# Performance work log

Measured on AMD Instinct MI355X. Metric: run time of the kernel, lower is better.

## Reference

```python
import jax, jax.numpy as jnp
import numpy as np

B, TC, TP = 2, 1024, 512
NVC, NVP = 8, 4
D, K, H, DFF, L, HOR, NQ = 128, 3, 8, 512, 2, 96, 3
DK = D // H
MASK_VAL = -1e4  # finite stand-in for -inf; entmax15 support never reaches entries this far below the row max


def entmax15(z):
    # Exact 1.5-entmax over the last axis (Peters & Martins sort-based algorithm).
    z = z / 2.0
    z = z - jnp.max(z, axis=-1, keepdims=True)
    zs = jnp.flip(jnp.sort(z, axis=-1), axis=-1)  # descending
    kk = jnp.arange(1, z.shape[-1] + 1, dtype=z.dtype)
    mean = jnp.cumsum(zs, axis=-1) / kk
    meansq = jnp.cumsum(zs * zs, axis=-1) / kk
    ss = kk * (meansq - mean * mean)
    delta = (1.0 - ss) / kk
    pos = delta > 0
    sqrt_d = jnp.where(pos, jnp.sqrt(jnp.where(pos, delta, 1.0)), 0.0)  # grad-safe sqrt
    tau = mean - sqrt_d
    support = jnp.sum((tau <= zs).astype(jnp.int32), axis=-1, keepdims=True)
    tau_star = jnp.take_along_axis(tau, support - 1, axis=-1)
    return jnp.square(jnp.clip(z - tau_star, 0.0, None))


def layer_norm(x, g, b, eps=1e-5):
    m = jnp.mean(x, axis=-1, keepdims=True)
    v = jnp.mean(jnp.square(x - m), axis=-1, keepdims=True)
    return (x - m) * jax.lax.rsqrt(v + eps) * g + b


def selector(x, conv_w, conv_b, sel_w, sel_b, key):
    # x: [B, T, nv]; causal depthwise-grouped conv -> per-var local states [B, T, nv, D]
    Bs, T, nv = x.shape
    xc = jnp.transpose(x, (0, 2, 1))  # [B, nv, T]
    out = jax.lax.conv_general_dilated(
        xc, conv_w, window_strides=(1,), padding=[(K - 1, 0)],
        dimension_numbers=('NCH', 'OIH', 'NCH'), feature_group_count=nv)
    ls = out.reshape(Bs, nv, D, T) + conv_b[None, :, :, None]
    ls = jnp.transpose(ls, (0, 3, 1, 2))  # [B, T, nv, D]
    scores = ls @ sel_w + sel_b  # [B, T, nv]
    scores = jnp.clip(scores, -10.0, 10.0)
    scores = scores + 1e-4 * jax.random.normal(key, scores.shape, scores.dtype)
    w = entmax15(scores)  # [B, T, nv]
    weighted = jnp.sum(ls * w[..., None], axis=2)  # [B, T, D]
    return weighted, w


def attn_block(x, Wq, bq, Wk, bk, Wv, bv, Wo, bo):
    Bs, T, _ = x.shape
    q = (x @ Wq + bq).reshape(Bs, T, H, DK)
    k = (x @ Wk + bk).reshape(Bs, T, H, DK)
    v = (x @ Wv + bv).reshape(Bs, T, H, DK)
    scores = jnp.einsum('bthd,bshd->bhts', q, k) / jnp.sqrt(jnp.float32(DK))
    mask = jnp.triu(jnp.ones((T, T), bool), 1)
    scores = jnp.where(mask[None, None], MASK_VAL, scores)
    w = entmax15(scores)            # [B, H, T, T]
    w_avg = jnp.mean(w, axis=1)     # [B, T, T]
    v_comb = jnp.mean(v, axis=2)    # [B, T, DK]
    out = jnp.einsum('bts,bsd->btd', w_avg, v_comb)
    return out @ Wo + bo, w_avg


def forward(x_cond, x_pred, cw_c, cb_c, sw_c, sb_c, cw_p, cb_p, sw_p, sb_p,
            Wq, bq, Wk, bk, Wv, bv, Wo, bo, ln1_g, ln1_b,
            fw1, fb1, fw2, fb2, ln2_g, ln2_b, proj_w, proj_b):
    nk = jax.random.key(42)
    xc, v_cond = selector(x_cond, cw_c, cb_c, sw_c, sb_c, jax.random.fold_in(nk, 0))
    xp, v_pred = selector(x_pred, cw_p, cb_p, sw_p, sb_p, jax.random.fold_in(nk, 1))
    x = jnp.concatenate([xc, xp], axis=1)  # [B, TC+TP, D]
    logs = []
    for l in range(L):
        a, w = attn_block(x, Wq[l], bq[l], Wk[l], bk[l], Wv[l], bv[l], Wo[l], bo[l])
        x = layer_norm(x + a, ln1_g[l], ln1_b[l])
        h = jax.nn.relu(x @ fw1[l] + fb1[l])
        x = layer_norm(h @ fw2[l] + fb2[l] + x, ln2_g[l], ln2_b[l])
        logs.append(w)
    seq_last = x[:, -1, :]
    out = jnp.einsum('bd,qdh->bqh', seq_last, proj_w) + proj_b  # [B, NQ, HOR]
    return out, v_cond, v_pred, jnp.stack(logs)


def setup_inputs():
    key = jax.random.key(0)
    ks = jax.random.split(key, 16)
    def w(i, shp):
        return (0.02 * jax.random.normal(ks[i], shp)).astype(jnp.float32)
    z = lambda shp: jnp.zeros(shp, jnp.float32)
    o = lambda shp: jnp.ones(shp, jnp.float32)
    return {
        'x_cond': jax.random.normal(ks[0], (B, TC, NVC), jnp.float32),
        'x_pred': jax.random.normal(ks[1], (B, TP, NVP), jnp.float32),
        'cw_c': w(2, (NVC * D, 1, K)), 'cb_c': z((NVC, D)),
        'sw_c': w(3, (D,)), 'sb_c': z((1,)),
        'cw_p': w(4, (NVP * D, 1, K)), 'cb_p': z((NVP, D)),
        'sw_p': w(5, (D,)), 'sb_p': z((1,)),
        'Wq': w(6, (L, D, D)), 'bq': z((L, D)),
        'Wk': w(7, (L, D, D)), 'bk': z((L, D)),
        'Wv': w(8, (L, D, D)), 'bv': z((L, D)),
        'Wo': w(9, (L, DK, D)), 'bo': z((L, D)),
        'ln1_g': o((L, D)), 'ln1_b': z((L, D)),
        'fw1': w(10, (L, D, DFF)), 'fb1': z((L, DFF)),
        'fw2': w(11, (L, DFF, D)), 'fb2': z((L, D)),
        'ln2_g': o((L, D)), 'ln2_b': z((L, D)),
        'proj_w': w(12, (NQ, D, HOR)), 'proj_b': z((NQ, HOR)),
    }


def reference(x_cond, x_pred, cw_c, cb_c, sw_c, sb_c, cw_p, cb_p, sw_p, sb_p,
              Wq, bq, Wk, bk, Wv, bv, Wo, bo, ln1_g, ln1_b,
              fw1, fb1, fw2, fb2, ln2_g, ln2_b, proj_w, proj_b):
    return forward(x_cond, x_pred, cw_c, cb_c, sw_c, sb_c, cw_p, cb_p, sw_p, sb_p,
                   Wq, bq, Wk, bk, Wv, bv, Wo, bo, ln1_g, ln1_b,
                   fw1, fb1, fw2, fb2, ln2_g, ln2_b, proj_w, proj_b)
```

## Files before the change

kernel.cpp:

```cpp
#include <hip/hip_runtime.h>

namespace {

constexpr int NB_  = 2;
constexpr int TC_  = 1024;
constexpr int TP_  = 512;
constexpr int TT_  = 1536;
constexpr int D_   = 128;
constexpr int H_   = 8;
constexpr int DK_  = 16;
constexpr int DFF_ = 512;
constexpr int L_   = 2;
constexpr int HOR_ = 96;
constexpr int NQ_  = 3;

constexpr int SCP_ = TT_ + 8;

typedef _Float16 h2 __attribute__((ext_vector_type(2)));

constexpr int OFF_OUT  = 0;
constexpr int OFF_VC   = NB_ * NQ_ * HOR_;
constexpr int OFF_VP   = OFF_VC + NB_ * TC_ * 8;
constexpr int OFF_LOGS = OFF_VP + NB_ * TP_ * 4;

constexpr int WS_XA  = 0;
constexpr int WS_XB  = WS_XA  + NB_ * TT_ * D_;
constexpr int WS_Q16 = WS_XB  + NB_ * TT_ * D_;
constexpr int WS_K16 = WS_Q16 + NB_ * TT_ * D_ / 2;
constexpr int WS_VC  = WS_K16 + NB_ * TT_ * D_ / 2;
constexpr int WS_WVC = WS_VC  + NB_ * TT_ * DK_;
constexpr int WS_BVC = WS_WVC + L_ * D_ * DK_;

__device__ inline float dot2f(h2 a, h2 b, float c) {
#if __has_builtin(__builtin_amdgcn_fdot2)
    return __builtin_amdgcn_fdot2(a, b, c, false);
#else
    return c + (float)a[0] * (float)b[0] + (float)a[1] * (float)b[1];
#endif
}

__device__ inline unsigned pack2h(float a, float b) {
#if __has_builtin(__builtin_amdgcn_cvt_pkrtz)
    return __builtin_bit_cast(unsigned, __builtin_amdgcn_cvt_pkrtz(a, b));
#else
    h2 p; p[0] = (_Float16)a; p[1] = (_Float16)b;
    return __builtin_bit_cast(unsigned, p);
#endif
}

__device__ inline float fast_rcp(float x) {
#if __has_builtin(__builtin_amdgcn_rcpf)
    return __builtin_amdgcn_rcpf(x);
#else
    return 1.0f / x;
#endif
}

template <int CTRL>
__device__ inline float dpp_add(float x) {
    const int y = __builtin_amdgcn_update_dpp(
        0, __builtin_bit_cast(int, x), CTRL, 0xF, 0xF, true);
    return x + __builtin_bit_cast(float, y);
}
template <int CTRL>
__device__ inline float dpp_maxf(float x) {
    const int y = __builtin_amdgcn_update_dpp(
        __builtin_bit_cast(int, x), __builtin_bit_cast(int, x),
        CTRL, 0xF, 0xF, false);
    return fmaxf(x, __builtin_bit_cast(float, y));
}
__device__ inline float bcast63(float x) {
    return __builtin_bit_cast(float,
        __builtin_amdgcn_readlane(__builtin_bit_cast(int, x), 63));
}
__device__ inline float wave_sum_l63(float x) {
    x = dpp_add<0x111>(x); x = dpp_add<0x112>(x); x = dpp_add<0x114>(x);
    x = dpp_add<0x118>(x); x = dpp_add<0x142>(x); x = dpp_add<0x143>(x);
    return x;
}
__device__ inline float wave_sum(float x) { return bcast63(wave_sum_l63(x)); }
__device__ inline float wave_max(float x) {
    x = dpp_maxf<0x111>(x); x = dpp_maxf<0x112>(x); x = dpp_maxf<0x114>(x);
    x = dpp_maxf<0x118>(x); x = dpp_maxf<0x142>(x); x = dpp_maxf<0x143>(x);
    return bcast63(x);
}

__global__ __launch_bounds__(128) void prep_wvc_kernel(
    const float* __restrict__ Wv, const float* __restrict__ bv,
    float* __restrict__ wvc, float* __restrict__ bvc)
{
    const int l = blockIdx.x;
    const float* W  = Wv + (long)l * D_ * D_;
    const float* bb = bv + l * D_;
    float* wv = wvc + l * D_ * DK_;
    float* bo = bvc + l * DK_;
    const int tid = threadIdx.x;
    for (int idx = tid; idx < D_ * DK_; idx += 128) {
        const int i = idx >> 4, dk = idx & 15;
        float s = 0.f;
        #pragma unroll
        for (int hh = 0; hh < H_; ++hh) s += W[i * D_ + hh * DK_ + dk];
        wv[idx] = s * 0.125f;
    }
    if (tid < DK_) {
        float s = 0.f;
        #pragma unroll
        for (int hh = 0; hh < H_; ++hh) s += bb[hh * DK_ + tid];
        bo[tid] = s * 0.125f;
    }
}

template <int NV>
__device__ inline void selector_qkv_body(
    const float* __restrict__ x, const float* __restrict__ cw,
    const float* __restrict__ cb, const float* __restrict__ sw,
    const float* __restrict__ sb, float* __restrict__ vout,
    float* __restrict__ xout, int Tsel, int row_off, int blk,
    const float* __restrict__ Wq, const float* __restrict__ bq,
    const float* __restrict__ Wk, const float* __restrict__ bk,
    const float* __restrict__ wvc, const float* __restrict__ bvc,
    _Float16* __restrict__ q16, _Float16* __restrict__ k16,
    float* __restrict__ vc)
{
    const int tpb = Tsel / 4;
    const int b   = blk / tpb;
    const int t0  = (blk - b * tpb) * 4;
    const int tid = threadIdx.x;
    const int lane = tid & 63, wave = tid >> 6;
    const int t = t0 + wave;

    __shared__ float xrT[D_][4];

    const int d0 = lane, d1 = lane + 64;
    float xw[3 * NV];
    #pragma unroll
    for (int kk = 0; kk < 3; ++kk) {
        const int ts = t + kk - 2;
        #pragma unroll
        for (int v = 0; v < NV; ++v)
            xw[kk * NV + v] = (ts >= 0) ? x[((long)b * Tsel + ts) * NV + v] : 0.0f;
    }
    float ls0[NV], ls1[NV];
    #pragma unroll
    for (int v = 0; v < NV; ++v) {
        const float* c0 = cw + ((long)(v * D_ + d0)) * 3;
        const float* c1 = cw + ((long)(v * D_ + d1)) * 3;
        float a0 = cb[v * D_ + d0], a1 = cb[v * D_ + d1];
        a0 = fmaf(xw[0*NV+v], c0[0], a0); a1 = fmaf(xw[0*NV+v], c1[0], a1);
        a0 = fmaf(xw[1*NV+v], c0[1], a0); a1 = fmaf(xw[1*NV+v], c1[1], a1);
        a0 = fmaf(xw[2*NV+v], c0[2], a0); a1 = fmaf(xw[2*NV+v], c1[2], a1);
        ls0[v] = a0; ls1[v] = a1;
    }
    float u[NV];
    {
        const float s0 = sw[d0], s1 = sw[d1];
        #pragma unroll
        for (int v = 0; v < NV; ++v)
            u[v] = wave_sum(fmaf(ls1[v], s1, ls0[v] * s0));
    }
    float wls[NV];
    {
        float m = -1e30f;
        #pragma unroll
        for (int v = 0; v < NV; ++v) {
            float s = u[v] + sb[0];
            s = fminf(fmaxf(s, -10.0f), 10.0f);
            u[v] = 0.5f * s;
            m = fmaxf(m, u[v]);
        }
        float tau = m - 1.0f;
        for (int it = 0; it < 12; ++it) {
            float S1 = 0.f, S2 = 0.f;
            #pragma unroll
            for (int v = 0; v < NV; ++v) {
                float dd = fmaxf(u[v] - tau, 0.f);
                S1 += dd; S2 = fmaf(dd, dd, S2);
            }
            tau += (S2 - 1.0f) * 0.5f * fast_rcp(S1);
        }
        float S1 = 0.f, S2 = 0.f, K = 0.f;
        #pragma unroll
        for (int v = 0; v < NV; ++v) {
            if (u[v] > tau) { S1 += u[v]; S2 = fmaf(u[v], u[v], S2); K += 1.f; }
        }
        const float mean = S1 / K;
        const float arg  = fmaxf(fmaf(mean, mean, -(S2 - 1.0f) / K), 0.f);
        tau = mean - sqrtf(arg);
        #pragma unroll
        for (int v = 0; v < NV; ++v) {
            const float dd = fmaxf(u[v] - tau, 0.f);
            wls[v] = dd * dd;
        }
    }
    float acc0 = 0.f, acc1 = 0.f;
    #pragma unroll
    for (int v = 0; v < NV; ++v) {
        acc0 = fmaf(ls0[v], wls[v], acc0);
        acc1 = fmaf(ls1[v], wls[v], acc1);
    }
    const long rowb = (long)b * TT_ + row_off + t0;
    const long row  = rowb + wave;
    xout[row * D_ + d0] = acc0;
    xout[row * D_ + d1] = acc1;
    xrT[d0][wave] = acc0;
    xrT[d1][wave] = acc1;
    if (lane == 0) {
        #pragma unroll
        for (int v = 0; v < NV; ++v)
            vout[((long)b * Tsel + t) * NV + v] = wls[v];
    }
    __syncthreads();

    {
        const int c = tid & 127;
        const int which = tid >> 7;
        const float* __restrict__ W = which ? Wk : Wq;
        const float bb = which ? bk[c] : bq[c];
        float a0 = bb, a1 = bb, a2 = bb, a3 = bb;
        for (int i = 0; i < D_; ++i) {
            const float wv = W[i * D_ + c];
            const float4 xv = *(const float4*)&xrT[i][0];
            a0 = fmaf(xv.x, wv, a0);
            a1 = fmaf(xv.y, wv, a1);
            a2 = fmaf(xv.z, wv, a2);
            a3 = fmaf(xv.w, wv, a3);
        }
        _Float16* __restrict__ dst = which ? k16 : q16;
        dst[(rowb + 0) * D_ + c] = (_Float16)a0;
        dst[(rowb + 1) * D_ + c] = (_Float16)a1;
        dst[(rowb + 2) * D_ + c] = (_Float16)a2;
        dst[(rowb + 3) * D_ + c] = (_Float16)a3;
    }
    if (tid < 64) {
        const int r = tid >> 4, c16 = tid & 15;
        float av = bvc[c16];
        for (int i = 0; i < D_; ++i)
            av = fmaf(xrT[i][r], wvc[i * DK_ + c16], av);
        vc[(rowb + r) * DK_ + c16] = av;
    }
}

__global__ __launch_bounds__(256) void pre_kernel(
    const float* __restrict__ x_cond, const float* __restrict__ cw_c,
    const float* __restrict__ cb_c, const float* __restrict__ sw_c,
    const float* __restrict__ sb_c,
    const float* __restrict__ x_pred, const float* __restrict__ cw_p,
    const float* __restrict__ cb_p, const float* __restrict__ sw_p,
    const float* __restrict__ sb_p,
    float* __restrict__ vc_out, float* __restrict__ vp_out,
    float* __restrict__ xout,
    const float* __restrict__ Wq, const float* __restrict__ bq,
    const float* __restrict__ Wk, const float* __restrict__ bk,
    const float* __restrict__ wvc, const float* __restrict__ bvc,
    _Float16* __restrict__ q16, _Float16* __restrict__ k16,
    float* __restrict__ vc)
{
    const int blk = blockIdx.x;
    if (blk < NB_ * TC_ / 4) {
        selector_qkv_body<8>(x_cond, cw_c, cb_c, sw_c, sb_c, vc_out, xout,
                             TC_, 0, blk, Wq, bq, Wk, bk, wvc, bvc,
                             q16, k16, vc);
    } else {
        selector_qkv_body<4>(x_pred, cw_p, cb_p, sw_p, sb_p, vp_out, xout,
                             TP_, TC_, blk - NB_ * TC_ / 4,
                             Wq, bq, Wk, bk, wvc, bvc, q16, k16, vc);
    }
}

template <int NJ>
__device__ inline void entmax_head2(unsigned short* __restrict__ sa,
                                    unsigned short* __restrict__ sb,
                                    int lane, int t)
{
    const unsigned* __restrict__ rpa = (const unsigned*)sa;
    const unsigned* __restrict__ rpb = (const unsigned*)sb;
    float va[2 * NJ], vb[2 * NJ];
    #pragma unroll
    for (int j = 0; j < NJ; ++j) {
        const unsigned dwa = rpa[64 * j + lane];
        const unsigned dwb = rpb[64 * j + lane];
        const h2 ha = __builtin_bit_cast(h2, dwa);
        const h2 hb = __builtin_bit_cast(h2, dwb);
        const int s0 = 128 * j + 2 * lane;
        const bool in0 = (s0 <= t), in1 = (s0 + 1 <= t);
        va[2*j]   = in0 ? (float)ha[0] : -1e30f;
        va[2*j+1] = in1 ? (float)ha[1] : -1e30f;
        vb[2*j]   = in0 ? (float)hb[0] : -1e30f;
        vb[2*j+1] = in1 ? (float)hb[1] : -1e30f;
    }

    float ma0 = va[0], ma1 = va[1], mb0 = vb[0], mb1 = vb[1];
    #pragma unroll
    for (int j = 2; j < 2 * NJ; j += 2) {
        ma0 = fmaxf(ma0, va[j]); ma1 = fmaxf(ma1, va[j+1]);
        mb0 = fmaxf(mb0, vb[j]); mb1 = fmaxf(mb1, vb[j+1]);
    }
    const float ma = wave_max(fmaxf(ma0, ma1));
    const float mb = wave_max(fmaxf(mb0, mb1));

    float ta = ma - 1.0f, tb = mb - 1.0f;
    #pragma unroll
    for (int it = 0; it < 7; ++it) {
        float a10 = 0.f, a11 = 0.f, a20 = 0.f, a21 = 0.f;
        float b10 = 0.f, b11 = 0.f, b20 = 0.f, b21 = 0.f;
        #pragma unroll
        for (int j = 0; j < 2 * NJ; j += 2) {
            const float da0 = fmaxf(va[j]   - ta, 0.f);
            const float da1 = fmaxf(va[j+1] - ta, 0.f);
            const float db0 = fmaxf(vb[j]   - tb, 0.f);
            const float db1 = fmaxf(vb[j+1] - tb, 0.f);
            a10 += da0; a11 += da1;
            a20 = fmaf(da0, da0, a20); a21 = fmaf(da1, da1, a21);
            b10 += db0; b11 += db1;
            b20 = fmaf(db0, db0, b20); b21 = fmaf(db1, db1, b21);
        }
        const float S1a = wave_sum(a10 + a11);
        const float S2a = wave_sum(a20 + a21);
        const float S1b = wave_sum(b10 + b11);
        const float S2b = wave_sum(b20 + b21);
        ta += (S2a - 1.0f) * 0.5f * fast_rcp(S1a);
        tb += (S2b - 1.0f) * 0.5f * fast_rcp(S1b);
    }
    {
        float a1 = 0.f, a2 = 0.f, ka = 0.f;
        float b1 = 0.f, b2 = 0.f, kb = 0.f;
        #pragma unroll
        for (int j = 0; j < 2 * NJ; ++j) {
            if (va[j] > ta) { a1 += va[j]; a2 = fmaf(va[j], va[j], a2); ka += 1.f; }
            if (vb[j] > tb) { b1 += vb[j]; b2 = fmaf(vb[j], vb[j], b2); kb += 1.f; }
        }
        a1 = wave_sum(a1); a2 = wave_sum(a2); ka = wave_sum(ka);
        b1 = wave_sum(b1); b2 = wave_sum(b2); kb = wave_sum(kb);
        const float meana = a1 / ka;
        const float arga  = fmaxf(fmaf(meana, meana, -(a2 - 1.0f) / ka), 0.f);
        ta = meana - sqrtf(arga);
        const float meanb = b1 / kb;
        const float argb  = fmaxf(fmaf(meanb, meanb, -(b2 - 1.0f) / kb), 0.f);
        tb = meanb - sqrtf(argb);
    }
    unsigned* __restrict__ wpa = (unsigned*)sa;
    unsigned* __restrict__ wpb = (unsigned*)sb;
    #pragma unroll
    for (int j = 0; j < NJ; ++j) {
        const float da0 = fmaxf(va[2*j]   - ta, 0.f);
        const float da1 = fmaxf(va[2*j+1] - ta, 0.f);
        const float db0 = fmaxf(vb[2*j]   - tb, 0.f);
        const float db1 = fmaxf(vb[2*j+1] - tb, 0.f);
        wpa[64 * j + lane] = pack2h(da0 * da0, da1 * da1);
        wpb[64 * j + lane] = pack2h(db0 * db0, db1 * db1);
    }
}

template <int NJ>
__device__ inline void entmax_pair(unsigned short* __restrict__ scb,
                                   int wave, int lane, int t)
{
    entmax_head2<NJ>(scb + (wave * 2 + 0) * SCP_,
                     scb + (wave * 2 + 1) * SCP_, lane, t);
}

__global__ __launch_bounds__(256) void attn_kernel(
    const _Float16* __restrict__ q16, const _Float16* __restrict__ k16,
    const float* __restrict__ vcomb, const float* __restrict__ xin,
    float* __restrict__ xout,
    const float* __restrict__ Wo, const float* __restrict__ bo,
    const float* __restrict__ lng, const float* __restrict__ lnb,
    float* __restrict__ logs)
{
    __shared__ unsigned short scb[H_ * SCP_];
    __shared__ _Float16 qrow16[D_];
    __shared__ float red[64];
    __shared__ float o16[DK_];
    __shared__ float yrow[D_];
    __shared__ float stat[2];

    const int blk = blockIdx.x;
    const int t = TT_ - 1 - (blk >> 1);
    const int b = blk & 1;
    const int tid = threadIdx.x;
    const int lane = tid & 63, wave = tid >> 6;
    const long rowq  = (long)b * TT_ + t;
    const long bbase = (long)b * TT_;

    if (tid < 64)
        ((unsigned*)qrow16)[tid] = ((const unsigned*)(q16 + rowq * D_))[tid];
    __syncthreads();

    {
        const int h  = tid & 7;
        const int sl = tid >> 3;
        unsigned short* __restrict__ srow = scb + h * SCP_;
        h2 qv[8];
        __builtin_memcpy(qv, (const _Float16*)qrow16 + h * DK_, 32);
        for (int s = sl; s <= t; s += 32) {
            float4 kk0, kk1;
            {
                const float4* kp4 = (const float4*)(k16 + (bbase + s) * D_ + h * DK_);
                kk0 = kp4[0]; kk1 = kp4[1];
            }
            h2 kh[8];
            __builtin_memcpy(kh,     &kk0, 16);
            __builtin_memcpy(kh + 4, &kk1, 16);
            float dot = 0.f;
            #pragma unroll
            for (int i2 = 0; i2 < 8; ++i2) dot = dot2f(qv[i2], kh[i2], dot);
            const _Float16 sh = (_Float16)(dot * 0.125f);
            srow[s] = __builtin_bit_cast(unsigned short, sh);
        }
    }
    __syncthreads();

    {
        const int njn = (t >> 7) + 1;
        switch ((njn + 1) & ~1) {
        case 2:  entmax_pair<2 >(scb, wave, lane, t); break;
        case 4:  entmax_pair<4 >(scb, wave, lane, t); break;
        case 6:  entmax_pair<6 >(scb, wave, lane, t); break;
        case 8:  entmax_pair<8 >(scb, wave, lane, t); break;
        case 10: entmax_pair<10>(scb, wave, lane, t); break;
        default: entmax_pair<12>(scb, wave, lane, t); break;
        }
    }
    __syncthreads();

    float4 A0 = make_float4(0,0,0,0), A1 = A0, A2 = A0, A3 = A0;
    float* lrow = logs + rowq * TT_;
    const unsigned* __restrict__ rp0 = (const unsigned*)scb;
    #pragma unroll
    for (int it = 0; it < 3; ++it) {
        const int dwi = tid + 256 * it;
        const int s0 = 2 * dwi;
        if (s0 <= t) {
            h2 hs = __builtin_bit_cast(h2, rp0[dwi]);
            #pragma unroll
            for (int h = 1; h < H_; ++h)
                hs = hs + __builtin_bit_cast(h2, rp0[h * (SCP_ / 2) + dwi]);
            const float wa0 = (float)hs[0] * 0.125f;
            const float wa1 = (float)hs[1] * 0.125f;
            {
                const float4* vp = (const float4*)(vcomb + (bbase + s0) * DK_);
                const float4 v0 = vp[0], v1 = vp[1], v2 = vp[2], v3 = vp[3];
                A0.x = fmaf(wa0, v0.x, A0.x); A0.y = fmaf(wa0, v0.y, A0.y);
                A0.z = fmaf(wa0, v0.z, A0.z); A0.w = fmaf(wa0, v0.w, A0.w);
                A1.x = fmaf(wa0, v1.x, A1.x); A1.y = fmaf(wa0, v1.y, A1.y);
                A1.z = fmaf(wa0, v1.z, A1.z); A1.w = fmaf(wa0, v1.w, A1.w);
                A2.x = fmaf(wa0, v2.x, A2.x); A2.y = fmaf(wa0, v2.y, A2.y);
                A2.z = fmaf(wa0, v2.z, A2.z); A2.w = fmaf(wa0, v2.w, A2.w);
                A3.x = fmaf(wa0, v3.x, A3.x); A3.y = fmaf(wa0, v3.y, A3.y);
                A3.z = fmaf(wa0, v3.z, A3.z); A3.w = fmaf(wa0, v3.w, A3.w);
            }
            if (s0 + 1 <= t) {
                const float4* vp = (const float4*)(vcomb + (bbase + s0 + 1) * DK_);
                const float4 v0 = vp[0], v1 = vp[1], v2 = vp[2], v3 = vp[3];
                A0.x = fmaf(wa1, v0.x, A0.x); A0.y = fmaf(wa1, v0.y, A0.y);
                A0.z = fmaf(wa1, v0.z, A0.z); A0.w = fmaf(wa1, v0.w, A0.w);
                A1.x = fmaf(wa1, v1.x, A1.x); A1.y = fmaf(wa1, v1.y, A1.y);
                A1.z = fmaf(wa1, v1.z, A1.z); A1.w = fmaf(wa1, v1.w, A1.w);
                A2.x = fmaf(wa1, v2.x, A2.x); A2.y = fmaf(wa1, v2.y, A2.y);
                A2.z = fmaf(wa1, v2.z, A2.z); A2.w = fmaf(wa1, v2.w, A2.w);
                A3.x = fmaf(wa1, v3.x, A3.x); A3.y = fmaf(wa1, v3.y, A3.y);
                A3.z = fmaf(wa1, v3.z, A3.z); A3.w = fmaf(wa1, v3.w, A3.w);
            }
            *(float2*)(lrow + s0) = make_float2(wa0, wa1);
        } else {
            *(float2*)(lrow + s0) = make_float2(0.f, 0.f);
        }
    }
    A0.x = wave_sum_l63(A0.x); A0.y = wave_sum_l63(A0.y);
    A0.z = wave_sum_l63(A0.z); A0.w = wave_sum_l63(A0.w);
    A1.x = wave_sum_l63(A1.x); A1.y = wave_sum_l63(A1.y);
    A1.z = wave_sum_l63(A1.z); A1.w = wave_sum_l63(A1.w);
    A2.x = wave_sum_l63(A2.x); A2.y = wave_sum_l63(A2.y);
    A2.z = wave_sum_l63(A2.z); A2.w = wave_sum_l63(A2.w);
    A3.x = wave_sum_l63(A3.x); A3.y = wave_sum_l63(A3.y);
    A3.z = wave_sum_l63(A3.z); A3.w = wave_sum_l63(A3.w);
    if (lane == 63) {
        float* r = red + wave * 16;
        r[0]=A0.x; r[1]=A0.y; r[2]=A0.z; r[3]=A0.w;
        r[4]=A1.x; r[5]=A1.y; r[6]=A1.z; r[7]=A1.w;
        r[8]=A2.x; r[9]=A2.y; r[10]=A2.z; r[11]=A2.w;
        r[12]=A3.x; r[13]=A3.y; r[14]=A3.z; r[15]=A3.w;
    }
    __syncthreads();
    if (tid < DK_) o16[tid] = red[tid] + red[16 + tid] + red[32 + tid] + red[48 + tid];
    __syncthreads();

    float y = 0.f;
    if (tid < D_) {
        float a = bo[tid];
        #pragma unroll
        for (int j = 0; j < DK_; ++j) a = fmaf(o16[j], Wo[j * D_ + tid], a);
        y = xin[rowq * D_ + tid] + a;
        yrow[tid] = y;
    }
    __syncthreads();
    if (tid < 64) {
        const float y0 = yrow[tid], y1 = yrow[tid + 64];
        float sm = wave_sum_l63(y0 + y1);
        float sq = wave_sum_l63(fmaf(y0, y0, y1 * y1));
        if (tid == 63) {
            const float mean = sm * (1.0f / D_);
            stat[0] = mean;
            stat[1] = fmaxf(sq * (1.0f / D_) - mean * mean, 0.f);
        }
    }
    __syncthreads();
    if (tid < D_) {
        const float r = rsqrtf(stat[1] + 1e-5f);
        xout[rowq * D_ + tid] = (y - stat[0]) * r * lng[tid] + lnb[tid];
    }
}

__global__ __launch_bounds__(256) void ffn_kernel(
    const float* __restrict__ xin, float* __restrict__ xout,
    const float* __restrict__ fw1, const float* __restrict__ fb1,
    const float* __restrict__ fw2, const float* __restrict__ fb2,
    const float* __restrict__ g, const float* __restrict__ bta,
    int do_qkv,
    const float* __restrict__ Wq, const float* __restrict__ bq,
    const float* __restrict__ Wk, const float* __restrict__ bk,
    const float* __restrict__ wvc, const float* __restrict__ bvc,
    _Float16* __restrict__ q16, _Float16* __restrict__ k16,
    float* __restrict__ vc,
    int do_proj, const float* __restrict__ pw,
    const float* __restrict__ pb, float* __restrict__ outp)
{
    __shared__ float xrT[D_][4];
    __shared__ float hbT[DFF_][4];
    __shared__ float pred[2][4][D_];
    __shared__ float xn[D_];

    const long row0 = (long)blockIdx.x * 4;
    const int tid = threadIdx.x;

    for (int idx = tid; idx < 4 * D_; idx += 256) {
        const int r = idx >> 7, i = idx & 127;
        xrT[i][r] = xin[row0 * D_ + idx];
    }
    __syncthreads();

    {
        const int c = tid;
        float4 a0 = make_float4(0,0,0,0), a1 = a0;
        for (int i = 0; i < D_; ++i) {
            const float w0 = fw1[i * DFF_ + c];
            const float w1 = fw1[i * DFF_ + c + 256];
            const float4 xv = *(const float4*)&xrT[i][0];
            a0.x = fmaf(xv.x, w0, a0.x); a0.y = fmaf(xv.y, w0, a0.y);
            a0.z = fmaf(xv.z, w0, a0.z); a0.w = fmaf(xv.w, w0, a0.w);
            a1.x = fmaf(xv.x, w1, a1.x); a1.y = fmaf(xv.y, w1, a1.y);
            a1.z = fmaf(xv.z, w1, a1.z); a1.w = fmaf(xv.w, w1, a1.w);
        }
        const float b0 = fb1[c], b1 = fb1[c + 256];
        float4 h0, h1;
        h0.x = fmaxf(a0.x + b0, 0.f); h0.y = fmaxf(a0.y + b0, 0.f);
        h0.z = fmaxf(a0.z + b0, 0.f); h0.w = fmaxf(a0.w + b0, 0.f);
        h1.x = fmaxf(a1.x + b1, 0.f); h1.y = fmaxf(a1.y + b1, 0.f);
        h1.z = fmaxf(a1.z + b1, 0.f); h1.w = fmaxf(a1.w + b1, 0.f);
        *(float4*)&hbT[c][0]       = h0;
        *(float4*)&hbT[c + 256][0] = h1;
    }
    __syncthreads();

    {
        const int d = tid & 127;
        const int half = tid >> 7;
        const int j0 = half * 256;
        float a0 = 0.f, a1 = 0.f, a2 = 0.f, a3 = 0.f;
        for (int j = j0; j < j0 + 256; ++j) {
            const float wv = fw2[j * D_ + d];
            const float4 hv = *(const float4*)&hbT[j][0];
            a0 = fmaf(hv.x, wv, a0);
            a1 = fmaf(hv.y, wv, a1);
            a2 = fmaf(hv.z, wv, a2);
            a3 = fmaf(hv.w, wv, a3);
        }
        pred[half][0][d] = a0; pred[half][1][d] = a1;
        pred[half][2][d] = a2; pred[half][3][d] = a3;
    }
    __syncthreads();

    const int w = tid >> 6, lane = tid & 63;
    const bool pblk = do_proj && (((row0 + 4) % TT_) == 0);
    {
        const float y0 = pred[0][w][lane]      + pred[1][w][lane]
                       + fb2[lane]             + xrT[lane][w];
        const float y1 = pred[0][w][lane + 64] + pred[1][w][lane + 64]
                       + fb2[lane + 64]        + xrT[lane + 64][w];
        const float sm = wave_sum(y0 + y1);
        const float sq = wave_sum(fmaf(y0, y0, y1 * y1));
        const float mean = sm * (1.0f / D_);
        const float var  = fmaxf(sq * (1.0f / D_) - mean * mean, 0.f);
        const float rcp = rsqrtf(var + 1e-5f);
        const float o0 = (y0 - mean) * rcp * g[lane]      + bta[lane];
        const float o1 = (y1 - mean) * rcp * g[lane + 64] + bta[lane + 64];
        xout[(row0 + w) * D_ + lane]      = o0;
        xout[(row0 + w) * D_ + lane + 64] = o1;
        xrT[lane][w]      = o0;
        xrT[lane + 64][w] = o1;
        if (pblk && w == 3) { xn[lane] = o0; xn[lane + 64] = o1; }
    }

    if (do_qkv) {
        __syncthreads();
        const int c = tid & 127;
        const int which = tid >> 7;
        const float* __restrict__ W = which ? Wk : Wq;
        const float bb = which ? bk[c] : bq[c];
        float a0 = bb, a1 = bb, a2 = bb, a3 = bb;
        for (int i = 0; i < D_; ++i) {
            const float wv = W[i * D_ + c];
            const float4 xv = *(const float4*)&xrT[i][0];
            a0 = fmaf(xv.x, wv, a0);
            a1 = fmaf(xv.y, wv, a1);
            a2 = fmaf(xv.z, wv, a2);
            a3 = fmaf(xv.w, wv, a3);
        }
        _Float16* __restrict__ dst = which ? k16 : q16;
        dst[(row0 + 0) * D_ + c] = (_Float16)a0;
        dst[(row0 + 1) * D_ + c] = (_Float16)a1;
        dst[(row0 + 2) * D_ + c] = (_Float16)a2;
        dst[(row0 + 3) * D_ + c] = (_Float16)a3;

        if (tid < 64) {
            const int r = tid >> 4, c16 = tid & 15;
            float av = bvc[c16];
            for (int i = 0; i < D_; ++i)
                av = fmaf(xrT[i][r], wvc[i * DK_ + c16], av);
            vc[(row0 + r) * DK_ + c16] = av;
        }
    }

    if (pblk) {
        __syncthreads();
        const int b = (int)((row0 + 3) / TT_);
        for (int idx = tid; idx < NQ_ * HOR_; idx += 256) {
            const int qq = idx / HOR_, hh = idx - qq * HOR_;
            float s = pb[idx];
            for (int d = 0; d < D_; ++d)
                s = fmaf(xn[d], pw[((long)qq * D_ + d) * HOR_ + hh], s);
            outp[b * NQ_ * HOR_ + idx] = s;
        }
    }
}

}

extern "C" void kernel_launch(void* const* d_in, const int* in_sizes, int n_in,
                              void* d_out, int out_size, void* d_ws, size_t ws_size,
                              hipStream_t stream) {
    (void)in_sizes; (void)n_in; (void)out_size; (void)ws_size;

    const float* x_cond = (const float*)d_in[0];
    const float* x_pred = (const float*)d_in[1];
    const float* cw_c   = (const float*)d_in[2];
    const float* cb_c   = (const float*)d_in[3];
    const float* sw_c   = (const float*)d_in[4];
    const float* sb_c   = (const float*)d_in[5];
    const float* cw_p   = (const float*)d_in[6];
    const float* cb_p   = (const float*)d_in[7];
    const float* sw_p   = (const float*)d_in[8];
    const float* sb_p   = (const float*)d_in[9];
    const float* Wq     = (const float*)d_in[10];
    const float* bq     = (const float*)d_in[11];
    const float* Wk     = (const float*)d_in[12];
    const float* bk     = (const float*)d_in[13];
    const float* Wv     = (const float*)d_in[14];
    const float* bv     = (const float*)d_in[15];
    const float* Wo     = (const float*)d_in[16];
    const float* bo     = (const float*)d_in[17];
    const float* ln1g   = (const float*)d_in[18];
    const float* ln1b   = (const float*)d_in[19];
    const float* fw1    = (const float*)d_in[20];
    const float* fb1    = (const float*)d_in[21];
    const float* fw2    = (const float*)d_in[22];
    const float* fb2    = (const float*)d_in[23];
    const float* ln2g   = (const float*)d_in[24];
    const float* ln2b   = (const float*)d_in[25];
    const float* pw     = (const float*)d_in[26];
    const float* pb     = (const float*)d_in[27];

    float* outp = (float*)d_out;
    float* ws   = (float*)d_ws;
    float*     xA   = ws + WS_XA;
    float*     xB   = ws + WS_XB;
    _Float16*  q16  = (_Float16*)(ws + WS_Q16);
    _Float16*  k16  = (_Float16*)(ws + WS_K16);
    float*     vcb  = ws + WS_VC;
    float*     wvc  = ws + WS_WVC;
    float*     bvc  = ws + WS_BVC;

    prep_wvc_kernel<<<L_, 128, 0, stream>>>(Wv, bv, wvc, bvc);

    pre_kernel<<<(NB_ * TC_ + NB_ * TP_) / 4, 256, 0, stream>>>(
        x_cond, cw_c, cb_c, sw_c, sb_c,
        x_pred, cw_p, cb_p, sw_p, sb_p,
        outp + OFF_VC, outp + OFF_VP, xA,
        Wq, bq, Wk, bk, wvc, bvc, q16, k16, vcb);

    for (int l = 0; l < L_; ++l) {
        attn_kernel<<<NB_ * TT_, 256, 0, stream>>>(
            q16, k16, vcb, xA, xB,
            Wo + (long)l * DK_ * D_, bo + l * D_,
            ln1g + l * D_, ln1b + l * D_,
            outp + OFF_LOGS + (long)l * NB_ * TT_ * TT_);
        const int nl = l + 1;
        ffn_kernel<<<NB_ * TT_ / 4, 256, 0, stream>>>(
            xB, xA, fw1 + (long)l * D_ * DFF_, fb1 + l * DFF_,
            fw2 + (long)l * DFF_ * D_, fb2 + l * D_,
            ln2g + l * D_, ln2b + l * D_,
            (l < L_ - 1) ? 1 : 0,
            Wq + (long)nl * D_ * D_ * (l < L_ - 1),
            bq + nl * D_ * (l < L_ - 1),
            Wk + (long)nl * D_ * D_ * (l < L_ - 1),
            bk + nl * D_ * (l < L_ - 1),
            wvc + nl * D_ * DK_ * (l < L_ - 1),
            bvc + nl * DK_ * (l < L_ - 1),
            q16, k16, vcb,
            (l == L_ - 1) ? 1 : 0, pw, pb, outp);
    }
}
```

Baseline: 302.9 us.

## Run FFN matmuls on MFMA with prepacked fp16 weight fragments

A prep kernel now converts the two FFN weight matrices to fp16 and lays them out in MFMA 16x16x32 fragment order. The FFN kernel then computes both layers with matrix-core instructions instead of scalar fp32 FMAs, padding the 4-row tile to 16 rows in shared memory. This targets the scalar FMA cost and fp32 weight traffic of the FFN. In exchange it adds fp16 rounding of activations and weights and wastes three quarters of each MFMA on zero padding rows.

```diff
diff --git a/kernel.cpp b/kernel.cpp
--- a/kernel.cpp
+++ b/kernel.cpp
@@ -17,6 +17,8 @@
 constexpr int SCP_ = TT_ + 8;
 
 typedef _Float16 h2 __attribute__((ext_vector_type(2)));
+typedef _Float16 h8 __attribute__((ext_vector_type(8)));
+typedef float    f32x4 __attribute__((ext_vector_type(4)));
 
 constexpr int OFF_OUT  = 0;
 constexpr int OFF_VC   = NB_ * NQ_ * HOR_;
@@ -30,6 +32,9 @@
 constexpr int WS_VC  = WS_K16 + NB_ * TT_ * D_ / 2;
 constexpr int WS_WVC = WS_VC  + NB_ * TT_ * DK_;
 constexpr int WS_BVC = WS_WVC + L_ * D_ * DK_;
+constexpr int FHL_   = 32768;
+constexpr int WS_FH1 = WS_BVC + L_ * DK_;
+constexpr int WS_FH2 = WS_FH1 + L_ * FHL_;
 
 __device__ inline float dot2f(h2 a, h2 b, float c) {
 #if __has_builtin(__builtin_amdgcn_fdot2)
@@ -85,28 +90,51 @@
     return bcast63(x);
 }
 
-__global__ __launch_bounds__(128) void prep_wvc_kernel(
+__global__ __launch_bounds__(256) void prep_kernel(
     const float* __restrict__ Wv, const float* __restrict__ bv,
-    float* __restrict__ wvc, float* __restrict__ bvc)
+    float* __restrict__ wvc, float* __restrict__ bvc,
+    const float* __restrict__ fw1, const float* __restrict__ fw2,
+    unsigned* __restrict__ fh1, unsigned* __restrict__ fh2)
 {
-    const int l = blockIdx.x;
-    const float* W  = Wv + (long)l * D_ * D_;
-    const float* bb = bv + l * D_;
-    float* wv = wvc + l * D_ * DK_;
-    float* bo = bvc + l * DK_;
-    const int tid = threadIdx.x;
-    for (int idx = tid; idx < D_ * DK_; idx += 128) {
-        const int i = idx >> 4, dk = idx & 15;
+    const int gid = blockIdx.x * 256 + threadIdx.x;
+    const int stride = gridDim.x * 256;
+
+    for (int e = gid; e < L_ * D_ * DK_; e += stride) {
+        const int l = e / (D_ * DK_), rem = e - l * D_ * DK_;
+        const int i = rem >> 4, dk = rem & 15;
+        const float* W = Wv + (long)l * D_ * D_;
         float s = 0.f;
         #pragma unroll
         for (int hh = 0; hh < H_; ++hh) s += W[i * D_ + hh * DK_ + dk];
-        wv[idx] = s * 0.125f;
-    }
-    if (tid < DK_) {
+        wvc[e] = s * 0.125f;
+    }
+    for (int e = gid; e < L_ * DK_; e += stride) {
+        const int l = e / DK_, dk = e - l * DK_;
+        const float* bb = bv + l * D_;
         float s = 0.f;
         #pragma unroll
-        for (int hh = 0; hh < H_; ++hh) s += bb[hh * DK_ + tid];
-        bo[tid] = s * 0.125f;
+        for (int hh = 0; hh < H_; ++hh) s += bb[hh * DK_ + dk];
+        bvc[e] = s * 0.125f;
+    }
+    for (int e = gid; e < L_ * FHL_; e += stride) {
+        const int l = e >> 15, rem = e & 32767;
+        const int tile = rem >> 8, within = rem & 255;
+        const int lane = within >> 2, p = within & 3;
+        const int kt = tile >> 5, nt = tile & 31;
+        const int k = kt * 32 + 8 * (lane >> 4) + 2 * p;
+        const int n = nt * 16 + (lane & 15);
+        const float* W = fw1 + (long)l * D_ * DFF_;
+        fh1[e] = pack2h(W[k * DFF_ + n], W[(k + 1) * DFF_ + n]);
+    }
+    for (int e = gid; e < L_ * FHL_; e += stride) {
+        const int l = e >> 15, rem = e & 32767;
+        const int tile = rem >> 8, within = rem & 255;
+        const int lane = within >> 2, p = within & 3;
+        const int kt = tile >> 3, nt = tile & 7;
+        const int k = kt * 32 + 8 * (lane >> 4) + 2 * p;
+        const int n = nt * 16 + (lane & 15);
+        const float* W = fw2 + (long)l * DFF_ * D_;
+        fh2[e] = pack2h(W[k * D_ + n], W[(k + 1) * D_ + n]);
     }
 }
 
@@ -513,8 +541,8 @@
 
 __global__ __launch_bounds__(256) void ffn_kernel(
     const float* __restrict__ xin, float* __restrict__ xout,
-    const float* __restrict__ fw1, const float* __restrict__ fb1,
-    const float* __restrict__ fw2, const float* __restrict__ fb2,
+    const unsigned* __restrict__ fh1l, const float* __restrict__ fb1,
+    const unsigned* __restrict__ fh2l, const float* __restrict__ fb2,
     const float* __restrict__ g, const float* __restrict__ bta,
     int do_qkv,
     const float* __restrict__ Wq, const float* __restrict__ bq,
@@ -525,68 +553,79 @@
     int do_proj, const float* __restrict__ pw,
     const float* __restrict__ pb, float* __restrict__ outp)
 {
-    __shared__ float xrT[D_][4];
-    __shared__ float hbT[DFF_][4];
-    __shared__ float pred[2][4][D_];
-    __shared__ float xn[D_];
+    __shared__ float    xrT[D_][4];
+    __shared__ _Float16 xh16[16][136];
+    __shared__ _Float16 h16[16][520];
+    __shared__ float    predf[4][D_];
+    __shared__ float    xn[D_];
 
     const long row0 = (long)blockIdx.x * 4;
     const int tid = threadIdx.x;
+    const int w = tid >> 6, l = tid & 63;
 
     for (int idx = tid; idx < 4 * D_; idx += 256) {
         const int r = idx >> 7, i = idx & 127;
-        xrT[i][r] = xin[row0 * D_ + idx];
-    }
-    __syncthreads();
-
-    {
-        const int c = tid;
-        float4 a0 = make_float4(0,0,0,0), a1 = a0;
-        for (int i = 0; i < D_; ++i) {
-            const float w0 = fw1[i * DFF_ + c];
-            const float w1 = fw1[i * DFF_ + c + 256];
-            const float4 xv = *(const float4*)&xrT[i][0];
-            a0.x = fmaf(xv.x, w0, a0.x); a0.y = fmaf(xv.y, w0, a0.y);
-            a0.z = fmaf(xv.z, w0, a0.z); a0.w = fmaf(xv.w, w0, a0.w);
-            a1.x = fmaf(xv.x, w1, a1.x); a1.y = fmaf(xv.y, w1, a1.y);
-            a1.z = fmaf(xv.z, w1, a1.z); a1.w = fmaf(xv.w, w1, a1.w);
-        }
-        const float b0 = fb1[c], b1 = fb1[c + 256];
-        float4 h0, h1;
-        h0.x = fmaxf(a0.x + b0, 0.f); h0.y = fmaxf(a0.y + b0, 0.f);
-        h0.z = fmaxf(a0.z + b0, 0.f); h0.w = fmaxf(a0.w + b0, 0.f);
-        h1.x = fmaxf(a1.x + b1, 0.f); h1.y = fmaxf(a1.y + b1, 0.f);
-        h1.z = fmaxf(a1.z + b1, 0.f); h1.w = fmaxf(a1.w + b1, 0.f);
-        *(float4*)&hbT[c][0]       = h0;
-        *(float4*)&hbT[c + 256][0] = h1;
-    }
-    __syncthreads();
-
-    {
-        const int d = tid & 127;
-        const int half = tid >> 7;
-        const int j0 = half * 256;
-        float a0 = 0.f, a1 = 0.f, a2 = 0.f, a3 = 0.f;
-        for (int j = j0; j < j0 + 256; ++j) {
-            const float wv = fw2[j * D_ + d];
-            const float4 hv = *(const float4*)&hbT[j][0];
-            a0 = fmaf(hv.x, wv, a0);
-            a1 = fmaf(hv.y, wv, a1);
-            a2 = fmaf(hv.z, wv, a2);
-            a3 = fmaf(hv.w, wv, a3);
-        }
-        pred[half][0][d] = a0; pred[half][1][d] = a1;
-        pred[half][2][d] = a2; pred[half][3][d] = a3;
-    }
-    __syncthreads();
-
-    const int w = tid >> 6, lane = tid & 63;
+        const float v = xin[row0 * D_ + idx];
+        xrT[i][r] = v;
+        xh16[r][i] = (_Float16)v;
+    }
+    for (int idx = tid; idx < 12 * 64; idx += 256)
+        *(unsigned*)&xh16[4 + (idx >> 6)][2 * (idx & 63)] = 0u;
+    for (int idx = tid; idx < 12 * 256; idx += 256)
+        *(unsigned*)&h16[4 + (idx >> 8)][2 * (idx & 255)] = 0u;
+    __syncthreads();
+
+    {
+        const int arow = l & 15, ak = 8 * (l >> 4);
+        h8 af[4];
+        #pragma unroll
+        for (int kt = 0; kt < 4; ++kt)
+            af[kt] = *(const h8*)&xh16[arow][kt * 32 + ak];
+        #pragma unroll
+        for (int nt8 = 0; nt8 < 8; ++nt8) {
+            const int nt = w * 8 + nt8;
+            f32x4 acc = {0.f, 0.f, 0.f, 0.f};
+            #pragma unroll
+            for (int kt = 0; kt < 4; ++kt) {
+                const h8 bf = *(const h8*)(fh1l + (((kt * 32 + nt) * 64 + l) << 2));
+                acc = __builtin_amdgcn_mfma_f32_16x16x32_f16(af[kt], bf, acc, 0, 0, 0);
+            }
+            if (l < 16) {
+                const int col = nt * 16 + l;
+                const float bias = fb1[col];
+                #pragma unroll
+                for (int j = 0; j < 4; ++j)
+                    h16[j][col] = (_Float16)fmaxf(acc[j] + bias, 0.f);
+            }
+        }
+    }
+    __syncthreads();
+
+    {
+        const int arow = l & 15, ak = 8 * (l >> 4);
+        f32x4 acc0 = {0.f, 0.f, 0.f, 0.f}, acc1 = acc0;
+        for (int kt = 0; kt < 16; ++kt) {
+            const h8 af = *(const h8*)&h16[arow][kt * 32 + ak];
+            const h8 b0 = *(const h8*)(fh2l + (((kt * 8 + 2 * w + 0) * 64 + l) << 2));
+            const h8 b1 = *(const h8*)(fh2l + (((kt * 8 + 2 * w + 1) * 64 + l) << 2));
+            acc0 = __builtin_amdgcn_mfma_f32_16x16x32_f16(af, b0, acc0, 0, 0, 0);
+            acc1 = __builtin_amdgcn_mfma_f32_16x16x32_f16(af, b1, acc1, 0, 0, 0);
+        }
+        if (l < 16) {
+            #pragma unroll
+            for (int j = 0; j < 4; ++j) {
+                predf[j][(2 * w + 0) * 16 + l] = acc0[j];
+                predf[j][(2 * w + 1) * 16 + l] = acc1[j];
+            }
+        }
+    }
+    __syncthreads();
+
+    const int lane = l;
     const bool pblk = do_proj && (((row0 + 4) % TT_) == 0);
     {
-        const float y0 = pred[0][w][lane]      + pred[1][w][lane]
-                       + fb2[lane]             + xrT[lane][w];
-        const float y1 = pred[0][w][lane + 64] + pred[1][w][lane + 64]
-                       + fb2[lane + 64]        + xrT[lane + 64][w];
+        const float y0 = predf[w][lane]      + fb2[lane]      + xrT[lane][w];
+        const float y1 = predf[w][lane + 64] + fb2[lane + 64] + xrT[lane + 64][w];
         const float sm = wave_sum(y0 + y1);
         const float sq = wave_sum(fmaf(y0, y0, y1 * y1));
         const float mean = sm * (1.0f / D_);
@@ -689,8 +728,11 @@
     float*     vcb  = ws + WS_VC;
     float*     wvc  = ws + WS_WVC;
     float*     bvc  = ws + WS_BVC;
-
-    prep_wvc_kernel<<<L_, 128, 0, stream>>>(Wv, bv, wvc, bvc);
+    unsigned*  fh1  = (unsigned*)(ws + WS_FH1);
+    unsigned*  fh2  = (unsigned*)(ws + WS_FH2);
+
+    prep_kernel<<<128, 256, 0, stream>>>(Wv, bv, wvc, bvc,
+                                         fw1, fw2, fh1, fh2);
 
     pre_kernel<<<(NB_ * TC_ + NB_ * TP_) / 4, 256, 0, stream>>>(
         x_cond, cw_c, cb_c, sw_c, sb_c,
@@ -706,8 +748,8 @@
             outp + OFF_LOGS + (long)l * NB_ * TT_ * TT_);
         const int nl = l + 1;
         ffn_kernel<<<NB_ * TT_ / 4, 256, 0, stream>>>(
-            xB, xA, fw1 + (long)l * D_ * DFF_, fb1 + l * DFF_,
-            fw2 + (long)l * DFF_ * D_, fb2 + l * D_,
+            xB, xA, fh1 + (long)l * FHL_, fb1 + l * DFF_,
+            fh2 + (long)l * FHL_, fb2 + l * D_,
             ln2g + l * D_, ln2b + l * D_,
             (l < L_ - 1) ? 1 : 0,
             Wq + (long)nl * D_ * D_ * (l < L_ - 1),
```

New measurement: 285.1 us. 1.06x faster.
